# Kernel optimization log

Hardware: AMD Instinct MI355X
Metric: run time of the kernel (lower is better)

Reference implementation:

```python
import jax, jax.numpy as jnp
import numpy as np

N_NODES = 100000
N_EDGES = 1600000
HID = 128
N_CONV = 3  # num_layers - 1
OUT_DIM = 1
BN_EPS = 1e-5


def _batchnorm(z, gamma, beta):
    # training-mode BN over node dim (batch statistics, biased variance)
    mean = jnp.mean(z, axis=0)
    var = jnp.mean((z - mean) ** 2, axis=0)
    return (z - mean) * jax.lax.rsqrt(var + BN_EPS) * gamma + beta


def setup_inputs() -> dict:
    key = jax.random.key(0)
    ks = jax.random.split(key, 16)
    s = 0.05
    inp = {
        "x": jax.random.randint(ks[0], (N_NODES,), 0, 2, dtype=jnp.int32),
        "edge_index": jax.random.randint(ks[1], (2, N_EDGES), 0, N_NODES, dtype=jnp.int64),
        "emb": jax.random.normal(ks[2], (2, HID), jnp.float32) * s,
        "W1": jax.random.normal(ks[3], (N_CONV, HID, HID), jnp.float32) * s,
        "W2": jax.random.normal(ks[4], (N_CONV, HID, HID), jnp.float32) * s,
        "bn1_g": jnp.ones((N_CONV, HID), jnp.float32),
        "bn1_b": jnp.zeros((N_CONV, HID), jnp.float32),
        "bn2_g": jnp.ones((N_CONV, HID), jnp.float32),
        "bn2_b": jnp.zeros((N_CONV, HID), jnp.float32),
        "rW1": jax.random.normal(ks[5], (4 * HID, HID), jnp.float32) * s,
        "rb1": jnp.zeros((HID,), jnp.float32),
        "rW2": jax.random.normal(ks[6], (HID, OUT_DIM), jnp.float32) * s,
        "rb2": jnp.zeros((OUT_DIM,), jnp.float32),
    }
    return inp


def reference(x, edge_index, emb, W1, W2, bn1_g, bn1_b, bn2_g, bn2_b, rW1, rb1, rW2, rb2):
    n = x.shape[0]
    src, dst = edge_index[0], edge_index[1]
    h = emb[x]  # [N, HID]
    reps = [h]
    for i in range(N_CONV):
        # GINConv: mlp((1+eps)*h + sum_{j in N(i)} h_j), eps=0
        agg = jax.ops.segment_sum(h[src], dst, num_segments=n)
        z = h + agg
        z = jnp.einsum('nd,df->nf', z, W1[i])
        z = jax.nn.relu(_batchnorm(z, bn1_g[i], bn1_b[i]))
        z = jnp.einsum('nd,df->nf', z, W2[i])
        z = _batchnorm(z, bn2_g[i], bn2_b[i])  # PyG BatchNorm after conv
        h = jax.nn.elu(z)
        reps.append(h)
    cat = jnp.concatenate(reps, axis=-1)  # [N, 4*HID]
    hid = jax.nn.relu(cat @ rW1 + rb1)
    return hid @ rW2 + rb2  # [N, OUT_DIM]
```

## Files before the change

### kernel.cpp

```cpp
#include <hip/hip_runtime.h>
#include <hip/hip_fp16.h>
#include <cstdint>
#include <cstddef>

#define NN 100000
#define NE 1600000
#define HID 128
#define BN_EPS 1e-5f
#define NB_SCAN 98
#define BM 96
#define NBLK ((NN + BM - 1) / BM)
#define NBC  ((NN + 255) / 256)
#define SA 72
#define SC_CHUNKS 256
#define SC_RANGE (NN / 8)
#define SC_EPC (NE / SC_CHUNKS)

typedef __attribute__((ext_vector_type(8))) short bf16x8;
typedef __attribute__((ext_vector_type(4))) float f32x4;
typedef __attribute__((ext_vector_type(4))) unsigned short u16x4;

static constexpr size_t SZ_NODE = (size_t)NN * HID * 4;
static constexpr size_t SZ_H16  = (size_t)NN * HID * 2;
static constexpr size_t OFF_P   = 0;
static constexpr size_t OFF_Q   = SZ_NODE;
static constexpr size_t OFF_R   = 2 * SZ_NODE;
static constexpr size_t OFF_CSR = 3 * SZ_NODE;
static constexpr size_t OFF_RP  = OFF_CSR + (size_t)NE * 4;
static constexpr size_t OFF_ZZ  = ((OFF_RP + (size_t)(NN + 1) * 4 + 255) / 256) * 256;
static constexpr size_t OFF_CNT = OFF_ZZ;
static constexpr size_t OFF_BS  = OFF_CNT + (((size_t)NN * 4 + 255) / 256) * 256;
static constexpr size_t OFF_FLG = OFF_BS + 512;
static constexpr size_t OFF_SS  = OFF_FLG + 256;
static constexpr size_t OFF_SCT = OFF_SS + 5 * 256 * 4;
static constexpr size_t ZZ_END  = ((OFF_SCT + 5 * 4 + 255) / 256) * 256;
static constexpr size_t ZZ_BYTES = ZZ_END - OFF_ZZ;
static constexpr size_t OFF_AC  = ZZ_END;
static constexpr size_t OFF_E   = OFF_AC + 6 * 256 * 4;
static constexpr size_t OFF_WSP = OFF_E + 512 * 4;
static constexpr size_t WS_NEEDED = OFF_WSP + (size_t)8 * 2 * HID * HID * 2;

__device__ __forceinline__ unsigned short f2bf(float f) {
  unsigned u = __float_as_uint(f);
  unsigned r = (u + 0x7fffu + ((u >> 16) & 1u)) >> 16;
  return (unsigned short)r;
}
__device__ __forceinline__ float bf2f(unsigned short b) {
  return __uint_as_float(((unsigned)b) << 16);
}
__device__ __forceinline__ int edge_at(const int* __restrict__ E, int f, int idx) {
  return f ? E[2 * (long long)idx] : E[idx];
}

__global__ void k_detect(const int* __restrict__ E, int* __restrict__ flag) {
  if (threadIdx.x == 0 && blockIdx.x == 0) {
    int f = 1;
    for (int i = 1; i < 256; i += 2)
      if (E[i] != 0) { f = 0; break; }
    *flag = f;
  }
}

__global__ __launch_bounds__(256) void k_hist(const int* __restrict__ E,
                                              const int* __restrict__ flag,
                                              int* __restrict__ cnt) {
  const int f = *flag;
  const int r = blockIdx.x & 7;
  const int chunk = blockIdx.x >> 3;
  const int lo = r * SC_RANGE, hi = lo + SC_RANGE;
  const int ebeg = chunk * SC_EPC, eend = ebeg + SC_EPC;
  for (int e = ebeg + threadIdx.x; e < eend; e += 256) {
    int d = edge_at(E, f, NE + e);
    d = min(max(d, 0), NN - 1);
    if (d >= lo && d < hi) atomicAdd(&cnt[d], 1);
  }
}

__global__ __launch_bounds__(256) void k_scan1(const int* __restrict__ cnt,
                                               int* __restrict__ rp,
                                               int* __restrict__ bs) {
  __shared__ int s[256];
  const int tid = threadIdx.x;
  const int base = blockIdx.x * 1024 + tid * 4;
  int v0 = 0, v1 = 0, v2 = 0, v3 = 0;
  if (base + 0 < NN) v0 = cnt[base + 0];
  if (base + 1 < NN) v1 = cnt[base + 1];
  if (base + 2 < NN) v2 = cnt[base + 2];
  if (base + 3 < NN) v3 = cnt[base + 3];
  const int t0 = v0, t1 = t0 + v1, t2 = t1 + v2, t3 = t2 + v3;
  s[tid] = t3;
  __syncthreads();
  for (int off = 1; off < 256; off <<= 1) {
    int xv = 0;
    if (tid >= off) xv = s[tid - off];
    __syncthreads();
    if (tid >= off) s[tid] += xv;
    __syncthreads();
  }
  const int excl = tid ? s[tid - 1] : 0;
  if (base + 0 < NN) rp[base + 0] = excl;
  if (base + 1 < NN) rp[base + 1] = excl + t0;
  if (base + 2 < NN) rp[base + 2] = excl + t1;
  if (base + 3 < NN) rp[base + 3] = excl + t2;
  if (tid == 255) bs[blockIdx.x] = s[255];
}

__global__ __launch_bounds__(128) void k_scan2(int* __restrict__ bs) {
  __shared__ int s[128];
  const int tid = threadIdx.x;
  s[tid] = (tid < NB_SCAN) ? bs[tid] : 0;
  __syncthreads();
  for (int off = 1; off < 128; off <<= 1) {
    int xv = 0;
    if (tid >= off) xv = s[tid - off];
    __syncthreads();
    if (tid >= off) s[tid] += xv;
    __syncthreads();
  }
  if (tid < NB_SCAN) bs[tid] = tid ? s[tid - 1] : 0;
}

__global__ __launch_bounds__(256) void k_scan3(int* __restrict__ rp,
                                               const int* __restrict__ bs,
                                               int* __restrict__ cursor) {
  const int off = bs[blockIdx.x];
  const int base = blockIdx.x * 1024 + threadIdx.x * 4;
  #pragma unroll
  for (int j = 0; j < 4; ++j) {
    const int i = base + j;
    if (i < NN) {
      const int v = rp[i] + off;
      rp[i] = v;
      cursor[i] = v;
    }
  }
  if (blockIdx.x == 0 && threadIdx.x == 0) rp[NN] = NE;
}

__global__ __launch_bounds__(256) void k_scatter(const int* __restrict__ E,
                                                 const int* __restrict__ flag,
                                                 int* __restrict__ cursor,
                                                 int* __restrict__ csr) {
  const int f = *flag;
  const int r = blockIdx.x & 7;
  const int chunk = blockIdx.x >> 3;
  const int lo = r * SC_RANGE, hi = lo + SC_RANGE;
  const int ebeg = chunk * SC_EPC, eend = ebeg + SC_EPC;
  for (int e = ebeg + threadIdx.x; e < eend; e += 256) {
    int d = edge_at(E, f, NE + e);
    d = min(max(d, 0), NN - 1);
    if (d >= lo && d < hi) {
      int s = edge_at(E, f, e);
      s = min(max(s, 0), NN - 1);
      const int pos = atomicAdd(&cursor[d], 1);
      if ((unsigned)pos < (unsigned)NE) csr[pos] = s;
    }
  }
}

__global__ __launch_bounds__(256) void k_prepw(const float* __restrict__ W1,
                                               const float* __restrict__ W2,
                                               const float* __restrict__ rW1,
                                               short* __restrict__ wsp) {
  const int g = blockIdx.x * 256 + threadIdx.x;
  const int m = g >> 14, idx = g & 16383;
  const int k = idx >> 7, n = idx & 127;
  const float* src;
  switch (m) {
    case 0: src = W2; break;
    case 1: src = W1 + 1 * HID * HID; break;
    case 2: src = W2 + 1 * HID * HID; break;
    case 3: src = W1 + 2 * HID * HID; break;
    case 4: src = W2 + 2 * HID * HID; break;
    case 5: src = rW1 + 1 * HID * HID; break;
    case 6: src = rW1 + 2 * HID * HID; break;
    default: src = rW1 + 3 * HID * HID; break;
  }
  const float v = src[k * HID + n];
  const unsigned short hb = f2bf(v);
  short* dst = wsp + (size_t)m * 32768;
  dst[n * HID + k] = (short)hb;
  dst[16384 + n * HID + k] = (short)f2bf(v - bf2f(hb));
}

__global__ __launch_bounds__(256) void k_prep(const float* __restrict__ emb,
                                              const float* __restrict__ W1,
                                              const float* __restrict__ rW1,
                                              float* __restrict__ ee) {
  const int t = threadIdx.x;
  const int f = t & 127;
  const float* er = emb + (t >> 7) * HID;
  float se = 0.f, sr = 0.f;
  for (int k = 0; k < HID; ++k) {
    const float ev = er[k];
    se = fmaf(ev, W1[k * HID + f], se);
    sr = fmaf(ev, rW1[k * HID + f], sr);
  }
  ee[t] = se;
  ee[256 + t] = sr;
}

__global__ __launch_bounds__(256) void k_cnt(const int* __restrict__ x,
                                             const int* __restrict__ rp,
                                             const int* __restrict__ csr,
                                             int* __restrict__ a01,
                                             float* __restrict__ momp) {
  const int n = blockIdx.x * 256 + threadIdx.x;
  float m[5] = {0.f, 0.f, 0.f, 0.f, 0.f};
  if (n < NN) {
    const int beg = rp[n], end = rp[n + 1];
    int c1 = 0;
    for (int j = beg; j < end; ++j) c1 += x[csr[j]] & 1;
    const int a1 = c1 + (x[n] & 1);
    const int a0 = (end - beg + 1) - a1;
    a01[n] = a0 | (a1 << 16);
    m[0] = (float)a0;
    m[1] = (float)a1;
    m[2] = (float)a0 * (float)a0;
    m[3] = (float)a1 * (float)a1;
    m[4] = (float)a0 * (float)a1;
  }
  #pragma unroll
  for (int j = 0; j < 5; ++j)
    #pragma unroll
    for (int off = 1; off < 64; off <<= 1) m[j] += __shfl_xor(m[j], off);
  __shared__ float sm[5][4];
  const int lane = threadIdx.x & 63, wv = threadIdx.x >> 6;
  if (lane == 0)
    #pragma unroll
    for (int j = 0; j < 5; ++j) sm[j][wv] = m[j];
  __syncthreads();
  if (threadIdx.x == 0)
    #pragma unroll
    for (int j = 0; j < 5; ++j)
      momp[j * NBC + blockIdx.x] = sm[j][0] + sm[j][1] + sm[j][2] + sm[j][3];
}

__global__ __launch_bounds__(128) void k_bnmom(const float* __restrict__ momp,
                                               const float* __restrict__ ee,
                                               const float* __restrict__ g,
                                               const float* __restrict__ b,
                                               float* __restrict__ a,
                                               float* __restrict__ c) {
  __shared__ float red[5][128];
  const int t = threadIdx.x;
  float s[5] = {0.f, 0.f, 0.f, 0.f, 0.f};
  for (int i = t; i < NBC; i += 128)
    #pragma unroll
    for (int j = 0; j < 5; ++j) s[j] += momp[j * NBC + i];
  #pragma unroll
  for (int j = 0; j < 5; ++j) red[j][t] = s[j];
  __syncthreads();
  for (int off = 64; off; off >>= 1) {
    if (t < off)
      #pragma unroll
      for (int j = 0; j < 5; ++j) red[j][t] += red[j][t + off];
    __syncthreads();
  }
  const float S0 = red[0][0], S1 = red[1][0];
  const float S00 = red[2][0], S11 = red[3][0], S01 = red[4][0];
  const float inv_n = 1.0f / (float)NN;
  const float e0 = ee[t], e1 = ee[128 + t];
  const float mean = (S0 * e0 + S1 * e1) * inv_n;
  const float msq = (S00 * e0 * e0 + 2.f * S01 * e0 * e1 + S11 * e1 * e1) * inv_n;
  float var = fmaxf(msq - mean * mean, 0.f);
  const float rs = rsqrtf(var + BN_EPS);
  const float av = g[t] * rs;
  a[t] = av;
  c[t] = b[t] - mean * av;
}

__global__ __launch_bounds__(256) void k_l1expand(const int* __restrict__ a01,
                                                  const float* __restrict__ ee,
                                                  float* __restrict__ u1) {
  const int total = NN * 32;
  for (int i = blockIdx.x * blockDim.x + threadIdx.x; i < total;
       i += gridDim.x * blockDim.x) {
    const int node = i >> 5, q = i & 31;
    const int p = a01[node];
    const float a0 = (float)(p & 0xffff), a1 = (float)(p >> 16);
    const float4 e0q = ((const float4*)ee)[q];
    const float4 e1q = ((const float4*)ee)[32 + q];
    float4 u;
    u.x = a0 * e0q.x + a1 * e1q.x;
    u.y = a0 * e0q.y + a1 * e1q.y;
    u.z = a0 * e0q.z + a1 * e1q.z;
    u.w = a0 * e0q.w + a1 * e1q.w;
    ((float4*)(u1 + (size_t)node * HID))[q] = u;
  }
}

__global__ __launch_bounds__(256) void k_agg(const __half* __restrict__ h,
                                             const int* __restrict__ rp,
                                             const int* __restrict__ csr,
                                             float* __restrict__ z) {
  const int wid = blockIdx.x * 4 + (threadIdx.x >> 6);
  const int lane = threadIdx.x & 63;
  if (wid >= NN) return;
  const int beg = rp[wid], end = rp[wid + 1];
  float2 acc = __half22float2(*((const __half2*)(h + (size_t)wid * HID) + lane));
  for (int j = beg; j < end; j += 64) {
    const int cnt = min(64, end - j);
    int idx = (lane < cnt) ? csr[j + lane] : 0;
    idx = min(max(idx, 0), NN - 1);
    int k = 0;
    for (; k + 4 <= cnt; k += 4) {
      const int s0 = __shfl(idx, k + 0), s1 = __shfl(idx, k + 1);
      const int s2 = __shfl(idx, k + 2), s3 = __shfl(idx, k + 3);
      const float2 v0 = __half22float2(*((const __half2*)(h + (size_t)s0 * HID) + lane));
      const float2 v1 = __half22float2(*((const __half2*)(h + (size_t)s1 * HID) + lane));
      const float2 v2 = __half22float2(*((const __half2*)(h + (size_t)s2 * HID) + lane));
      const float2 v3 = __half22float2(*((const __half2*)(h + (size_t)s3 * HID) + lane));
      acc.x += (v0.x + v1.x) + (v2.x + v3.x);
      acc.y += (v0.y + v1.y) + (v2.y + v3.y);
    }
    for (; k < cnt; ++k) {
      const int s = __shfl(idx, k);
      const float2 v = __half22float2(*((const __half2*)(h + (size_t)s * HID) + lane));
      acc.x += v.x;
      acc.y += v.y;
    }
  }
  *(float2*)(z + (size_t)wid * HID + lane * 2) = acc;
}

template <int IN_ACT, int OUT_MODE>
__global__ __launch_bounds__(256, 4) void k_gemm(
    float* A, const short* __restrict__ Wsp,
    const float* __restrict__ ina, const float* __restrict__ inc,
    float* __restrict__ out, float* __restrict__ part) {
  __shared__ short Ah[BM * SA];
  __shared__ short Al[BM * SA];
  const int tid = threadIdx.x;
  const int lane = tid & 63, wv = tid >> 6;
  const int tq = lane >> 4, tl = lane & 15;
  const int wc = wv * 32;
  const int m0 = blockIdx.x * BM;

  f32x4 acc[6][2];
  #pragma unroll
  for (int i = 0; i < 6; ++i)
    #pragma unroll
    for (int j = 0; j < 2; ++j) acc[i][j] = (f32x4)(0.f);

  for (int kt = 0; kt < HID; kt += 64) {
    if (kt) __syncthreads();
    #pragma unroll
    for (int p = 0; p < 6; ++p) {
      const int flat = p * 256 + tid;
      const int m = flat >> 4, kq = flat & 15;
      const int gm = m0 + m, gk = kt + kq * 4;
      float vv[4] = {0.f, 0.f, 0.f, 0.f};
      if (gm < NN) {
        const float4 v = *(const float4*)(A + (size_t)gm * HID + gk);
        vv[0] = v.x; vv[1] = v.y; vv[2] = v.z; vv[3] = v.w;
        if (IN_ACT == 1) {
          const float4 a4 = *(const float4*)(ina + gk);
          const float4 c4 = *(const float4*)(inc + gk);
          vv[0] = fmaxf(fmaf(vv[0], a4.x, c4.x), 0.f);
          vv[1] = fmaxf(fmaf(vv[1], a4.y, c4.y), 0.f);
          vv[2] = fmaxf(fmaf(vv[2], a4.z, c4.z), 0.f);
          vv[3] = fmaxf(fmaf(vv[3], a4.w, c4.w), 0.f);
        }
      }
      u16x4 hh, ll;
      #pragma unroll
      for (int j = 0; j < 4; ++j) {
        const unsigned short hb = f2bf(vv[j]);
        hh[j] = hb;
        ll[j] = f2bf(vv[j] - bf2f(hb));
      }
      *(u16x4*)(&Ah[m * SA + kq * 4]) = hh;
      *(u16x4*)(&Al[m * SA + kq * 4]) = ll;
    }
    __syncthreads();
    #pragma unroll
    for (int kc = 0; kc < 64; kc += 32) {
      const int lo = kc + tq * 8;
      const int go = kt + lo;
      bf16x8 wh[2], wl[2];
      #pragma unroll
      for (int fn = 0; fn < 2; ++fn) {
        const int n = wc + fn * 16 + tl;
        wh[fn] = *(const bf16x8*)(Wsp + n * HID + go);
        wl[fn] = *(const bf16x8*)(Wsp + 16384 + n * HID + go);
      }
      #pragma unroll
      for (int fm = 0; fm < 6; ++fm) {
        const int r = (fm * 16 + tl) * SA + lo;
        const bf16x8 ah = *(const bf16x8*)(&Ah[r]);
        const bf16x8 al = *(const bf16x8*)(&Al[r]);
        #pragma unroll
        for (int fn = 0; fn < 2; ++fn) {
          acc[fm][fn] = __builtin_amdgcn_mfma_f32_16x16x32_bf16(ah, wh[fn], acc[fm][fn], 0, 0, 0);
          acc[fm][fn] = __builtin_amdgcn_mfma_f32_16x16x32_bf16(ah, wl[fn], acc[fm][fn], 0, 0, 0);
          acc[fm][fn] = __builtin_amdgcn_mfma_f32_16x16x32_bf16(al, wh[fn], acc[fm][fn], 0, 0, 0);
        }
      }
    }
  }

  #pragma unroll
  for (int fm = 0; fm < 6; ++fm) {
    #pragma unroll
    for (int reg = 0; reg < 4; ++reg) {
      const int row = m0 + fm * 16 + tq * 4 + reg;
      if (row < NN) {
        float* op = out + (size_t)row * HID + wc + tl;
        op[0] = acc[fm][0][reg];
        op[16] = acc[fm][1][reg];
      }
    }
  }
  if (OUT_MODE == 0) {
    #pragma unroll
    for (int fn = 0; fn < 2; ++fn) {
      float s = 0.f, q = 0.f;
      #pragma unroll
      for (int fm = 0; fm < 6; ++fm)
        #pragma unroll
        for (int reg = 0; reg < 4; ++reg) {
          const float v = acc[fm][fn][reg];
          s += v;
          q = fmaf(v, v, q);
        }
      s += __shfl_xor(s, 16); q += __shfl_xor(q, 16);
      s += __shfl_xor(s, 32); q += __shfl_xor(q, 32);
      if (lane < 16) {
        const int col = wc + fn * 16 + lane;
        part[(size_t)blockIdx.x * 256 + col] = s;
        part[(size_t)blockIdx.x * 256 + 128 + col] = q;
      }
    }
  }
}

__global__ __launch_bounds__(256, 4) void k_rdgemm(
    const __half* __restrict__ h1, const __half* __restrict__ h2,
    const __half* __restrict__ h3, const short* __restrict__ wsp,
    const int* __restrict__ x, const float* __restrict__ ee,
    const float* __restrict__ rb1, const float* __restrict__ rW2,
    const float* __restrict__ rb2, float* __restrict__ out) {
  __shared__ short Ah[BM * SA];
  __shared__ short Al[BM * SA];
  const int tid = threadIdx.x;
  const int lane = tid & 63, wv = tid >> 6;
  const int tq = lane >> 4, tl = lane & 15;
  const int wc = wv * 32;
  const int m0 = blockIdx.x * BM;

  f32x4 acc[6][2];
  #pragma unroll
  for (int i = 0; i < 6; ++i)
    #pragma unroll
    for (int j = 0; j < 2; ++j) acc[i][j] = (f32x4)(0.f);

  for (int t6 = 0; t6 < 6; ++t6) {
    const __half* hsrc = (t6 < 2) ? h1 : (t6 < 4) ? h2 : h3;
    const short* Ws = wsp + (size_t)(t6 >> 1) * 32768;
    const int kt = (t6 & 1) * 64;
    if (t6) __syncthreads();
    #pragma unroll
    for (int p = 0; p < 6; ++p) {
      const int flat = p * 256 + tid;
      const int m = flat >> 4, kq = flat & 15;
      const int gm = m0 + m, gk = kt + kq * 4;
      float vv[4] = {0.f, 0.f, 0.f, 0.f};
      if (gm < NN) {
        const __half2 x0 = *(const __half2*)(hsrc + (size_t)gm * HID + gk);
        const __half2 x1 = *(const __half2*)(hsrc + (size_t)gm * HID + gk + 2);
        const float2 f0 = __half22float2(x0);
        const float2 f1 = __half22float2(x1);
        vv[0] = f0.x; vv[1] = f0.y; vv[2] = f1.x; vv[3] = f1.y;
      }
      u16x4 hh, ll;
      #pragma unroll
      for (int j = 0; j < 4; ++j) {
        const unsigned short hb = f2bf(vv[j]);
        hh[j] = hb;
        ll[j] = f2bf(vv[j] - bf2f(hb));
      }
      *(u16x4*)(&Ah[m * SA + kq * 4]) = hh;
      *(u16x4*)(&Al[m * SA + kq * 4]) = ll;
    }
    __syncthreads();
    #pragma unroll
    for (int kc = 0; kc < 64; kc += 32) {
      const int lo = kc + tq * 8;
      const int go = kt + lo;
      bf16x8 wh[2], wl[2];
      #pragma unroll
      for (int fn = 0; fn < 2; ++fn) {
        const int n = wc + fn * 16 + tl;
        wh[fn] = *(const bf16x8*)(Ws + n * HID + go);
        wl[fn] = *(const bf16x8*)(Ws + 16384 + n * HID + go);
      }
      #pragma unroll
      for (int fm = 0; fm < 6; ++fm) {
        const int r = (fm * 16 + tl) * SA + lo;
        const bf16x8 ah = *(const bf16x8*)(&Ah[r]);
        const bf16x8 al = *(const bf16x8*)(&Al[r]);
        #pragma unroll
        for (int fn = 0; fn < 2; ++fn) {
          acc[fm][fn] = __builtin_amdgcn_mfma_f32_16x16x32_bf16(ah, wh[fn], acc[fm][fn], 0, 0, 0);
          acc[fm][fn] = __builtin_amdgcn_mfma_f32_16x16x32_bf16(ah, wl[fn], acc[fm][fn], 0, 0, 0);
          acc[fm][fn] = __builtin_amdgcn_mfma_f32_16x16x32_bf16(al, wh[fn], acc[fm][fn], 0, 0, 0);
        }
      }
    }
  }

  const int c0 = wc + tl, c1 = wc + 16 + tl;
  const float rb_0 = rb1[c0], rb_1 = rb1[c1];
  const float w2_0 = rW2[c0], w2_1 = rW2[c1];
  const float r0_0 = ee[256 + c0], r0_1 = ee[256 + c1];
  const float r1_0 = ee[384 + c0], r1_1 = ee[384 + c1];
  __syncthreads();
  float* rs = (float*)Ah;
  #pragma unroll
  for (int fm = 0; fm < 6; ++fm) {
    #pragma unroll
    for (int reg = 0; reg < 4; ++reg) {
      const int row = fm * 16 + tq * 4 + reg;
      const int grow = m0 + row;
      const int xv = (grow < NN) ? (x[grow] & 1) : 0;
      const float g0 = acc[fm][0][reg] + rb_0 + (xv ? r1_0 : r0_0);
      const float g1 = acc[fm][1][reg] + rb_1 + (xv ? r1_1 : r0_1);
      float p = fmaxf(g0, 0.f) * w2_0 + fmaxf(g1, 0.f) * w2_1;
      p += __shfl_xor(p, 1);
      p += __shfl_xor(p, 2);
      p += __shfl_xor(p, 4);
      p += __shfl_xor(p, 8);
      if (tl == 0) rs[row * 4 + wv] = p;
    }
  }
  __syncthreads();
  if (tid < BM) {
    const int grow = m0 + tid;
    if (grow < NN)
      out[grow] = rs[tid * 4 + 0] + rs[tid * 4 + 1] + rs[tid * 4 + 2] +
                  rs[tid * 4 + 3] + rb2[0];
  }
}

__global__ __launch_bounds__(256) void k_bnstat(const float* __restrict__ part,
                                                const float* __restrict__ g,
                                                const float* __restrict__ b,
                                                float* __restrict__ a,
                                                float* __restrict__ c,
                                                float* __restrict__ S,
                                                int* __restrict__ ctr) {
  const int tid = threadIdx.x;
  float acc = 0.f;
  for (int r = blockIdx.x; r < NBLK; r += 64) acc += part[(size_t)r * 256 + tid];
  atomicAdd(&S[tid], acc);
  __syncthreads();
  __threadfence();
  __shared__ int last;
  if (tid == 0) last = (atomicAdd(ctr, 1) == 63);
  __syncthreads();
  if (!last) return;
  __threadfence();
  const float tot = atomicAdd(&S[tid], 0.f);
  __shared__ float sm[256];
  sm[tid] = tot;
  __syncthreads();
  if (tid < 128) {
    const float inv_n = 1.0f / (float)NN;
    const float mean = sm[tid] * inv_n;
    float var = fmaxf(sm[tid + 128] * inv_n - mean * mean, 0.f);
    const float rs = rsqrtf(var + BN_EPS);
    const float av = g[tid] * rs;
    a[tid] = av;
    c[tid] = b[tid] - mean * av;
  }
}

__global__ __launch_bounds__(256) void k_act(const float* __restrict__ v,
                                             const float* __restrict__ a,
                                             const float* __restrict__ c,
                                             __half* __restrict__ h) {
  const int total = NN * 32;
  for (int i = blockIdx.x * blockDim.x + threadIdx.x; i < total;
       i += gridDim.x * blockDim.x) {
    const int node = i >> 5, q = i & 31;
    const float4 vv = *(const float4*)(v + (size_t)node * HID + q * 4);
    const float4 a4 = ((const float4*)a)[q];
    const float4 c4 = ((const float4*)c)[q];
    float z;
    float o0, o1, o2, o3;
    z = fmaf(vv.x, a4.x, c4.x); o0 = z > 0.f ? z : expm1f(z);
    z = fmaf(vv.y, a4.y, c4.y); o1 = z > 0.f ? z : expm1f(z);
    z = fmaf(vv.z, a4.z, c4.z); o2 = z > 0.f ? z : expm1f(z);
    z = fmaf(vv.w, a4.w, c4.w); o3 = z > 0.f ? z : expm1f(z);
    const __half2 p0 = __floats2half2_rn(o0, o1);
    const __half2 p1 = __floats2half2_rn(o2, o3);
    uint2 u;
    u.x = *reinterpret_cast<const unsigned*>(&p0);
    u.y = *reinterpret_cast<const unsigned*>(&p1);
    *(uint2*)(h + (size_t)node * HID + q * 4) = u;
  }
}

extern "C" void kernel_launch(void* const* d_in, const int* in_sizes, int n_in,
                              void* d_out, int out_size, void* d_ws,
                              size_t ws_size, hipStream_t stream) {
  if (ws_size < WS_NEEDED) return;

  const int* x = (const int*)d_in[0];
  const int* E = (const int*)d_in[1];
  const float* emb = (const float*)d_in[2];
  const float* W1 = (const float*)d_in[3];
  const float* W2 = (const float*)d_in[4];
  const float* bn1g = (const float*)d_in[5];
  const float* bn1b = (const float*)d_in[6];
  const float* bn2g = (const float*)d_in[7];
  const float* bn2b = (const float*)d_in[8];
  const float* rW1 = (const float*)d_in[9];
  const float* rb1 = (const float*)d_in[10];
  const float* rW2 = (const float*)d_in[11];
  const float* rb2 = (const float*)d_in[12];
  float* outp = (float*)d_out;

  char* ws = (char*)d_ws;
  float* P = (float*)(ws + OFF_P);
  float* Q = (float*)(ws + OFF_Q);
  float* R = (float*)(ws + OFF_R);
  int* csr = (int*)(ws + OFF_CSR);
  int* rp = (int*)(ws + OFF_RP);
  int* cnt = (int*)(ws + OFF_CNT);
  int* bs = (int*)(ws + OFF_BS);
  int* flag = (int*)(ws + OFF_FLG);
  float* SS = (float*)(ws + OFF_SS);
  int* SCT = (int*)(ws + OFF_SCT);
  float* ac = (float*)(ws + OFF_AC);
  float* ee = (float*)(ws + OFF_E);
  short* wsp = (short*)(ws + OFF_WSP);
  __half* h1 = (__half*)P;
  __half* h2 = (__half*)((char*)P + SZ_H16);
  __half* h3 = (__half*)R;
  float* part = R;
  int* a01 = (int*)((char*)P + (4 << 20));
  float* momp = (float*)((char*)P + (8 << 20));

  hipMemsetAsync(ws + OFF_ZZ, 0, ZZ_BYTES, stream);
  k_detect<<<1, 64, 0, stream>>>(E, flag);
  k_hist<<<SC_CHUNKS * 8, 256, 0, stream>>>(E, flag, cnt);
  k_scan1<<<NB_SCAN, 256, 0, stream>>>(cnt, rp, bs);
  k_scan2<<<1, 128, 0, stream>>>(bs);
  k_scan3<<<NB_SCAN, 256, 0, stream>>>(rp, bs, cnt);
  k_scatter<<<SC_CHUNKS * 8, 256, 0, stream>>>(E, flag, cnt, csr);
  k_prep<<<1, 256, 0, stream>>>(emb, W1, rW1, ee);
  k_prepw<<<512, 256, 0, stream>>>(W1, W2, rW1, wsp);

  float* a1 = ac + 0 * 256, *c1 = a1 + HID;
  float* a2 = ac + 1 * 256, *c2 = a2 + HID;

  k_cnt<<<NBC, 256, 0, stream>>>(x, rp, csr, a01, momp);
  k_bnmom<<<1, 128, 0, stream>>>(momp, ee, bn1g, bn1b, a1, c1);
  k_l1expand<<<2048, 256, 0, stream>>>(a01, ee, Q);
  k_gemm<1, 0><<<NBLK, 256, 0, stream>>>(Q, wsp + 0 * 32768, a1, c1, Q, part);
  k_bnstat<<<64, 256, 0, stream>>>(part, bn2g, bn2b, a2, c2, SS + 0 * 256, SCT + 0);
  k_act<<<2048, 256, 0, stream>>>(Q, a2, c2, h1);

  int inst = 1;
  for (int i = 1; i < 3; ++i) {
    float* b1a = ac + (2 * i) * 256, *b1c = b1a + HID;
    float* b2a = ac + (2 * i + 1) * 256, *b2c = b2a + HID;
    const int s1 = (i == 1) ? 1 : 3;
    const __half* hin = (i == 1) ? h1 : h2;
    k_agg<<<NN / 4, 256, 0, stream>>>(hin, rp, csr, Q);
    k_gemm<0, 0><<<NBLK, 256, 0, stream>>>(Q, wsp + (size_t)s1 * 32768,
                                           nullptr, nullptr, Q, part);
    k_bnstat<<<64, 256, 0, stream>>>(part, bn1g + i * HID, bn1b + i * HID, b1a,
                                     b1c, SS + inst * 256, SCT + inst);
    ++inst;
    k_gemm<1, 0><<<NBLK, 256, 0, stream>>>(Q, wsp + (size_t)(s1 + 1) * 32768,
                                           b1a, b1c, Q, part);
    k_bnstat<<<64, 256, 0, stream>>>(part, bn2g + i * HID, bn2b + i * HID, b2a,
                                     b2c, SS + inst * 256, SCT + inst);
    ++inst;
    k_act<<<2048, 256, 0, stream>>>(Q, b2a, b2c, (i == 1) ? h2 : h3);
  }

  k_rdgemm<<<NBLK, 256, 0, stream>>>(h1, h2, h3, wsp + (size_t)5 * 32768, x, ee,
                                     rb1, rW2, rb2, outp);
}
```

Before: 719.5 us.

## Fuse layer-1 expand into GEMM, pack x bit in CSR, use fp16 readout GEMM

Drops the separate layer-1 expand kernel: the first GEMM now builds its input rows on the fly from the per-node neighbour counts and the embedding projections, which avoids writing and re-reading a full node-by-feature float buffer. The scatter pass stores each source node's x bit in the top bit of its CSR entry, so the count kernel no longer gathers x at random, and the aggregation kernel masks that bit off. The readout GEMM now feeds the fp16 activations straight into f16 MFMAs against a scaled hi/lo fp16 split of the weights, using two MFMAs per tile instead of three bf16 ones and no per-element split of the activations. In exchange it uses a second accumulator set and lowers launch bounds occupancy from 4 to 3, and it relies on fp16 range and precision for the readout weights.

Measured after the change: 710.1 us. About the same (-1.3%).

```diff
diff --git a/kernel.cpp b/kernel.cpp
--- a/kernel.cpp
+++ b/kernel.cpp
@@ -17,6 +17,7 @@
 #define SC_EPC (NE / SC_CHUNKS)
 
 typedef __attribute__((ext_vector_type(8))) short bf16x8;
+typedef __attribute__((ext_vector_type(8))) _Float16 f16x8;
 typedef __attribute__((ext_vector_type(4))) float f32x4;
 typedef __attribute__((ext_vector_type(4))) unsigned short u16x4;
 
@@ -139,6 +140,7 @@
 
 __global__ __launch_bounds__(256) void k_scatter(const int* __restrict__ E,
                                                  const int* __restrict__ flag,
+                                                 const int* __restrict__ x,
                                                  int* __restrict__ cursor,
                                                  int* __restrict__ csr) {
   const int f = *flag;
@@ -152,8 +154,9 @@
     if (d >= lo && d < hi) {
       int s = edge_at(E, f, e);
       s = min(max(s, 0), NN - 1);
+      const int xb = x[s] & 1;
       const int pos = atomicAdd(&cursor[d], 1);
-      if ((unsigned)pos < (unsigned)NE) csr[pos] = s;
+      if ((unsigned)pos < (unsigned)NE) csr[pos] = s | (xb << 31);
     }
   }
 }
@@ -177,10 +180,18 @@
     default: src = rW1 + 3 * HID * HID; break;
   }
   const float v = src[k * HID + n];
-  const unsigned short hb = f2bf(v);
   short* dst = wsp + (size_t)m * 32768;
-  dst[n * HID + k] = (short)hb;
-  dst[16384 + n * HID + k] = (short)f2bf(v - bf2f(hb));
+  if (m < 5) {
+    const unsigned short hb = f2bf(v);
+    dst[n * HID + k] = (short)hb;
+    dst[16384 + n * HID + k] = (short)f2bf(v - bf2f(hb));
+  } else {
+    const __half hh = __float2half_rn(v);
+    const float rem = v - __half2float(hh);
+    const __half hl = __float2half_rn(rem * 2048.f);
+    dst[n * HID + k] = (short)__half_as_ushort(hh);
+    dst[16384 + n * HID + k] = (short)__half_as_ushort(hl);
+  }
 }
 
 __global__ __launch_bounds__(256) void k_prep(const float* __restrict__ emb,
@@ -210,7 +221,7 @@
   if (n < NN) {
     const int beg = rp[n], end = rp[n + 1];
     int c1 = 0;
-    for (int j = beg; j < end; ++j) c1 += x[csr[j]] & 1;
+    for (int j = beg; j < end; ++j) c1 += (int)(((unsigned)csr[j]) >> 31);
     const int a1 = c1 + (x[n] & 1);
     const int a0 = (end - beg + 1) - a1;
     a01[n] = a0 | (a1 << 16);
@@ -270,26 +281,6 @@
   c[t] = b[t] - mean * av;
 }
 
-__global__ __launch_bounds__(256) void k_l1expand(const int* __restrict__ a01,
-                                                  const float* __restrict__ ee,
-                                                  float* __restrict__ u1) {
-  const int total = NN * 32;
-  for (int i = blockIdx.x * blockDim.x + threadIdx.x; i < total;
-       i += gridDim.x * blockDim.x) {
-    const int node = i >> 5, q = i & 31;
-    const int p = a01[node];
-    const float a0 = (float)(p & 0xffff), a1 = (float)(p >> 16);
-    const float4 e0q = ((const float4*)ee)[q];
-    const float4 e1q = ((const float4*)ee)[32 + q];
-    float4 u;
-    u.x = a0 * e0q.x + a1 * e1q.x;
-    u.y = a0 * e0q.y + a1 * e1q.y;
-    u.z = a0 * e0q.z + a1 * e1q.z;
-    u.w = a0 * e0q.w + a1 * e1q.w;
-    ((float4*)(u1 + (size_t)node * HID))[q] = u;
-  }
-}
-
 __global__ __launch_bounds__(256) void k_agg(const __half* __restrict__ h,
                                              const int* __restrict__ rp,
                                              const int* __restrict__ csr,
@@ -301,8 +292,8 @@
   float2 acc = __half22float2(*((const __half2*)(h + (size_t)wid * HID) + lane));
   for (int j = beg; j < end; j += 64) {
     const int cnt = min(64, end - j);
-    int idx = (lane < cnt) ? csr[j + lane] : 0;
-    idx = min(max(idx, 0), NN - 1);
+    int idx = (lane < cnt) ? (csr[j + lane] & 0x7fffffff) : 0;
+    idx = min(idx, NN - 1);
     int k = 0;
     for (; k + 4 <= cnt; k += 4) {
       const int s0 = __shfl(idx, k + 0), s1 = __shfl(idx, k + 1);
@@ -328,7 +319,8 @@
 __global__ __launch_bounds__(256, 4) void k_gemm(
     float* A, const short* __restrict__ Wsp,
     const float* __restrict__ ina, const float* __restrict__ inc,
-    float* __restrict__ out, float* __restrict__ part) {
+    float* __restrict__ out, float* __restrict__ part,
+    const int* __restrict__ a01, const float* __restrict__ ee) {
   __shared__ short Ah[BM * SA];
   __shared__ short Al[BM * SA];
   const int tid = threadIdx.x;
@@ -352,9 +344,20 @@
       const int gm = m0 + m, gk = kt + kq * 4;
       float vv[4] = {0.f, 0.f, 0.f, 0.f};
       if (gm < NN) {
-        const float4 v = *(const float4*)(A + (size_t)gm * HID + gk);
-        vv[0] = v.x; vv[1] = v.y; vv[2] = v.z; vv[3] = v.w;
-        if (IN_ACT == 1) {
+        if (IN_ACT == 2) {
+          const int pk = a01[gm];
+          const float a0 = (float)(pk & 0xffff), a1 = (float)(pk >> 16);
+          const float4 e0q = *(const float4*)(ee + gk);
+          const float4 e1q = *(const float4*)(ee + 128 + gk);
+          vv[0] = a0 * e0q.x + a1 * e1q.x;
+          vv[1] = a0 * e0q.y + a1 * e1q.y;
+          vv[2] = a0 * e0q.z + a1 * e1q.z;
+          vv[3] = a0 * e0q.w + a1 * e1q.w;
+        } else {
+          const float4 v = *(const float4*)(A + (size_t)gm * HID + gk);
+          vv[0] = v.x; vv[1] = v.y; vv[2] = v.z; vv[3] = v.w;
+        }
+        if (IN_ACT >= 1) {
           const float4 a4 = *(const float4*)(ina + gk);
           const float4 c4 = *(const float4*)(inc + gk);
           vv[0] = fmaxf(fmaf(vv[0], a4.x, c4.x), 0.f);
@@ -435,25 +438,24 @@
   }
 }
 
-__global__ __launch_bounds__(256, 4) void k_rdgemm(
+__global__ __launch_bounds__(256, 3) void k_rdgemm(
     const __half* __restrict__ h1, const __half* __restrict__ h2,
     const __half* __restrict__ h3, const short* __restrict__ wsp,
     const int* __restrict__ x, const float* __restrict__ ee,
     const float* __restrict__ rb1, const float* __restrict__ rW2,
     const float* __restrict__ rb2, float* __restrict__ out) {
   __shared__ short Ah[BM * SA];
-  __shared__ short Al[BM * SA];
   const int tid = threadIdx.x;
   const int lane = tid & 63, wv = tid >> 6;
   const int tq = lane >> 4, tl = lane & 15;
   const int wc = wv * 32;
   const int m0 = blockIdx.x * BM;
 
-  f32x4 acc[6][2];
+  f32x4 ach[6][2], acl[6][2];
   #pragma unroll
   for (int i = 0; i < 6; ++i)
     #pragma unroll
-    for (int j = 0; j < 2; ++j) acc[i][j] = (f32x4)(0.f);
+    for (int j = 0; j < 2; ++j) { ach[i][j] = (f32x4)(0.f); acl[i][j] = (f32x4)(0.f); }
 
   for (int t6 = 0; t6 < 6; ++t6) {
     const __half* hsrc = (t6 < 2) ? h1 : (t6 < 4) ? h2 : h3;
@@ -465,46 +467,29 @@
       const int flat = p * 256 + tid;
       const int m = flat >> 4, kq = flat & 15;
       const int gm = m0 + m, gk = kt + kq * 4;
-      float vv[4] = {0.f, 0.f, 0.f, 0.f};
-      if (gm < NN) {
-        const __half2 x0 = *(const __half2*)(hsrc + (size_t)gm * HID + gk);
-        const __half2 x1 = *(const __half2*)(hsrc + (size_t)gm * HID + gk + 2);
-        const float2 f0 = __half22float2(x0);
-        const float2 f1 = __half22float2(x1);
-        vv[0] = f0.x; vv[1] = f0.y; vv[2] = f1.x; vv[3] = f1.y;
-      }
-      u16x4 hh, ll;
-      #pragma unroll
-      for (int j = 0; j < 4; ++j) {
-        const unsigned short hb = f2bf(vv[j]);
-        hh[j] = hb;
-        ll[j] = f2bf(vv[j] - bf2f(hb));
-      }
-      *(u16x4*)(&Ah[m * SA + kq * 4]) = hh;
-      *(u16x4*)(&Al[m * SA + kq * 4]) = ll;
+      u16x4 hv = (u16x4)(0);
+      if (gm < NN) hv = *(const u16x4*)((const unsigned short*)hsrc + (size_t)gm * HID + gk);
+      *(u16x4*)(&Ah[m * SA + kq * 4]) = hv;
     }
     __syncthreads();
     #pragma unroll
     for (int kc = 0; kc < 64; kc += 32) {
       const int lo = kc + tq * 8;
       const int go = kt + lo;
-      bf16x8 wh[2], wl[2];
+      f16x8 wh[2], wl[2];
       #pragma unroll
       for (int fn = 0; fn < 2; ++fn) {
         const int n = wc + fn * 16 + tl;
-        wh[fn] = *(const bf16x8*)(Ws + n * HID + go);
-        wl[fn] = *(const bf16x8*)(Ws + 16384 + n * HID + go);
+        wh[fn] = *(const f16x8*)(Ws + n * HID + go);
+        wl[fn] = *(const f16x8*)(Ws + 16384 + n * HID + go);
       }
       #pragma unroll
       for (int fm = 0; fm < 6; ++fm) {
-        const int r = (fm * 16 + tl) * SA + lo;
-        const bf16x8 ah = *(const bf16x8*)(&Ah[r]);
-        const bf16x8 al = *(const bf16x8*)(&Al[r]);
+        const f16x8 a = *(const f16x8*)(&Ah[(fm * 16 + tl) * SA + lo]);
         #pragma unroll
         for (int fn = 0; fn < 2; ++fn) {
-          acc[fm][fn] = __builtin_amdgcn_mfma_f32_16x16x32_bf16(ah, wh[fn], acc[fm][fn], 0, 0, 0);
-          acc[fm][fn] = __builtin_amdgcn_mfma_f32_16x16x32_bf16(ah, wl[fn], acc[fm][fn], 0, 0, 0);
-          acc[fm][fn] = __builtin_amdgcn_mfma_f32_16x16x32_bf16(al, wh[fn], acc[fm][fn], 0, 0, 0);
+          ach[fm][fn] = __builtin_amdgcn_mfma_f32_16x16x32_f16(a, wh[fn], ach[fm][fn], 0, 0, 0);
+          acl[fm][fn] = __builtin_amdgcn_mfma_f32_16x16x32_f16(a, wl[fn], acl[fm][fn], 0, 0, 0);
         }
       }
     }
@@ -515,6 +500,7 @@
   const float w2_0 = rW2[c0], w2_1 = rW2[c1];
   const float r0_0 = ee[256 + c0], r0_1 = ee[256 + c1];
   const float r1_0 = ee[384 + c0], r1_1 = ee[384 + c1];
+  const float LS = 1.0f / 2048.0f;
   __syncthreads();
   float* rs = (float*)Ah;
   #pragma unroll
@@ -524,8 +510,8 @@
       const int row = fm * 16 + tq * 4 + reg;
       const int grow = m0 + row;
       const int xv = (grow < NN) ? (x[grow] & 1) : 0;
-      const float g0 = acc[fm][0][reg] + rb_0 + (xv ? r1_0 : r0_0);
-      const float g1 = acc[fm][1][reg] + rb_1 + (xv ? r1_1 : r0_1);
+      const float g0 = ach[fm][0][reg] + acl[fm][0][reg] * LS + rb_0 + (xv ? r1_0 : r0_0);
+      const float g1 = ach[fm][1][reg] + acl[fm][1][reg] * LS + rb_1 + (xv ? r1_1 : r0_1);
       float p = fmaxf(g0, 0.f) * w2_0 + fmaxf(g1, 0.f) * w2_1;
       p += __shfl_xor(p, 1);
       p += __shfl_xor(p, 2);
@@ -649,7 +635,7 @@
   k_scan1<<<NB_SCAN, 256, 0, stream>>>(cnt, rp, bs);
   k_scan2<<<1, 128, 0, stream>>>(bs);
   k_scan3<<<NB_SCAN, 256, 0, stream>>>(rp, bs, cnt);
-  k_scatter<<<SC_CHUNKS * 8, 256, 0, stream>>>(E, flag, cnt, csr);
+  k_scatter<<<SC_CHUNKS * 8, 256, 0, stream>>>(E, flag, x, cnt, csr);
   k_prep<<<1, 256, 0, stream>>>(emb, W1, rW1, ee);
   k_prepw<<<512, 256, 0, stream>>>(W1, W2, rW1, wsp);
 
@@ -658,8 +644,8 @@
 
   k_cnt<<<NBC, 256, 0, stream>>>(x, rp, csr, a01, momp);
   k_bnmom<<<1, 128, 0, stream>>>(momp, ee, bn1g, bn1b, a1, c1);
-  k_l1expand<<<2048, 256, 0, stream>>>(a01, ee, Q);
-  k_gemm<1, 0><<<NBLK, 256, 0, stream>>>(Q, wsp + 0 * 32768, a1, c1, Q, part);
+  k_gemm<2, 0><<<NBLK, 256, 0, stream>>>(Q, wsp + 0 * 32768, a1, c1, Q, part,
+                                         a01, ee);
   k_bnstat<<<64, 256, 0, stream>>>(part, bn2g, bn2b, a2, c2, SS + 0 * 256, SCT + 0);
   k_act<<<2048, 256, 0, stream>>>(Q, a2, c2, h1);
 
@@ -671,12 +657,13 @@
     const __half* hin = (i == 1) ? h1 : h2;
     k_agg<<<NN / 4, 256, 0, stream>>>(hin, rp, csr, Q);
     k_gemm<0, 0><<<NBLK, 256, 0, stream>>>(Q, wsp + (size_t)s1 * 32768,
-                                           nullptr, nullptr, Q, part);
+                                           nullptr, nullptr, Q, part, nullptr,
+                                           nullptr);
     k_bnstat<<<64, 256, 0, stream>>>(part, bn1g + i * HID, bn1b + i * HID, b1a,
                                      b1c, SS + inst * 256, SCT + inst);
     ++inst;
     k_gemm<1, 0><<<NBLK, 256, 0, stream>>>(Q, wsp + (size_t)(s1 + 1) * 32768,
-                                           b1a, b1c, Q, part);
+                                           b1a, b1c, Q, part, nullptr, nullptr);
     k_bnstat<<<64, 256, 0, stream>>>(part, bn2g + i * HID, bn2b + i * HID, b2a,
                                      b2c, SS + inst * 256, SCT + inst);
     ++inst;
```
